# Optimization experiments

Hardware: AMD Instinct MI355X
Metric: run time of the kernel (lower is better)

Reference implementation:

```python
import jax, jax.numpy as jnp
import numpy as np

N_NODES, N_EDGES = 16384, 8192
IN_CH, HID_CH = 256, 256
ALPHA, BETA = -1.5, -0.5


def setup_inputs() -> dict:
    key = jax.random.key(0)
    k1, k2, k3, k4, k5, k6 = jax.random.split(key, 6)
    x_0 = jax.random.normal(k1, (N_NODES, IN_CH), dtype=jnp.float32)
    # binary incidence matrix (n_nodes, n_edges)
    incidence_1 = jax.random.randint(k2, (N_NODES, N_EDGES), 0, 2).astype(jnp.float32)
    # conv weights (torch Conv: x @ W then neighborhood @ .)
    W0 = jax.random.normal(k3, (IN_CH, HID_CH), dtype=jnp.float32) * 0.02
    W1 = jax.random.normal(k4, (HID_CH, HID_CH), dtype=jnp.float32) * 0.02
    # xavier_uniform biases of shape (1, hidden)
    gain = 1.414
    bound = gain * np.sqrt(6.0 / (1 + HID_CH)) * np.sqrt(3.0) / np.sqrt(3.0)  # xavier bound = gain*sqrt(6/(fan_in+fan_out))
    bound = gain * np.sqrt(6.0 / (1 + HID_CH))
    bias_0_to_1 = jax.random.uniform(k5, (1, HID_CH), minval=-bound, maxval=bound, dtype=jnp.float32)
    bias_1_to_0 = jax.random.uniform(k6, (1, HID_CH), minval=-bound, maxval=bound, dtype=jnp.float32)
    return {"x_0": x_0, "incidence_1": incidence_1, "W0": W0, "W1": W1,
            "bias_0_to_1": bias_0_to_1, "bias_1_to_0": bias_1_to_0}


def _normalize_incidence(B1):
    # edge/node cardinalities raised to alpha/beta
    edge_card = jnp.sum(B1, axis=0) ** ALPHA          # (n_edges,)
    node_card = jnp.sum(B1, axis=1) ** BETA           # (n_nodes,)
    mask = (B1 > 0).astype(B1.dtype)
    d0_inv = 1.0 / (mask @ edge_card)                 # (n_nodes,) per-node sum of incident edge_card
    d1_inv = 1.0 / (mask.T @ node_card)               # (n_edges,) per-edge sum of member node_card
    # B1_norm = D0_left^-1 @ B1 @ diag(edge_card)
    B1_norm = d0_inv[:, None] * B1 * edge_card[None, :]
    # B1T_norm = D1_left^-1 @ B1^T @ diag(node_card)
    B1T_norm = d1_inv[:, None] * B1.T * node_card[None, :]
    return B1_norm, B1T_norm


def reference(x_0, incidence_1, W0, W1, bias_0_to_1, bias_1_to_0):
    B1_norm, B1T_norm = _normalize_incidence(incidence_1)
    # node -> edge conv: x_1 = B1T_norm @ (x_0 @ W0) + b01
    x_1 = B1T_norm @ (x_0 @ W0) + bias_0_to_1        # (n_edges, hid)
    # edge -> node conv: x_0 = B1_norm @ (x_1 @ W1) + b10
    x_0_out = B1_norm @ (x_1 @ W1) + bias_1_to_0     # (n_nodes, hid)
    return jax.nn.relu(x_0_out), jax.nn.relu(x_1)
```

## Files before the change

### kernel.cpp

```cpp
#include <hip/hip_runtime.h>
#include <stdint.h>

#define NN 16384
#define NE 8192
#define CH 256
#define MM1_SPLIT 8
#define MM2_SPLIT 4

typedef __attribute__((ext_vector_type(8))) short bf16x8;
typedef __attribute__((ext_vector_type(4))) float f32x4;

__device__ __forceinline__ unsigned short f2bf(float f) {
  unsigned u = __float_as_uint(f);
  u += 0x7FFFu + ((u >> 16) & 1u);
  return (unsigned short)(u >> 16);
}
__device__ __forceinline__ void async_copy16(const void* gptr, void* lptr) {
  __builtin_amdgcn_global_load_lds((const __attribute__((address_space(1))) unsigned int*)gptr,
                                   (__attribute__((address_space(3))) unsigned int*)lptr,
                                   16, 0, 0);
}
__device__ __forceinline__ uint4 expand8(unsigned byte) {
  uint4 aw;
#pragma unroll
  for (int j = 0; j < 4; ++j) {
    unsigned lo = (byte >> (2 * j)) & 1u;
    unsigned hi = (byte >> (2 * j + 1)) & 1u;
    ((unsigned*)&aw)[j] = lo * 0x3F80u + hi * 0x3F800000u;
  }
  return aw;
}

__device__ __forceinline__ void transpose32(unsigned* x) {
  const unsigned masks[5] = {0x0000FFFFu, 0x00FF00FFu, 0x0F0F0F0Fu, 0x33333333u, 0x55555555u};
#pragma unroll
  for (int jj = 0; jj < 5; ++jj) {
    const int j = 16 >> jj;
    const unsigned m = masks[jj];
#pragma unroll
    for (int k = 0; k < 32; ++k) {
      if ((k & j) == 0) {
        unsigned t = ((x[k] >> j) ^ x[k + j]) & m;
        x[k] ^= (t << j);
        x[k + j] ^= t;
      }
    }
  }
}

__global__ void k0_transpose_w(const float* __restrict__ W0, const float* __restrict__ W1,
                               unsigned short* __restrict__ W0T, unsigned short* __restrict__ W1T) {
  const float* W = blockIdx.y ? W1 : W0;
  unsigned short* WT = blockIdx.y ? W1T : W0T;
  int n = blockIdx.x;
  int k = threadIdx.x;
  WT[n * CH + k] = f2bf(W[k * CH + n]);
}

__global__ void k1_pack_card(const float* __restrict__ B1, unsigned* __restrict__ pk1,
                             float* __restrict__ node_card) {
  int n = blockIdx.x;
  int t = threadIdx.x;
  const float4* p = (const float4*)(B1 + (size_t)n * NE + t * 32);
  unsigned w = 0;
#pragma unroll
  for (int jj = 0; jj < 8; ++jj) {
    float4 v = p[jj];
    w |= ((__float_as_uint(v.x) >> 23) & 1u) << (4 * jj);
    w |= ((__float_as_uint(v.y) >> 23) & 1u) << (4 * jj + 1);
    w |= ((__float_as_uint(v.z) >> 23) & 1u) << (4 * jj + 2);
    w |= ((__float_as_uint(v.w) >> 23) & 1u) << (4 * jj + 3);
  }
  pk1[(size_t)n * 256 + t] = w;
  int s = __popc(w);
  __shared__ int red[4];
#pragma unroll
  for (int off = 32; off; off >>= 1) s += __shfl_down(s, off, 64);
  if ((t & 63) == 0) red[t >> 6] = s;
  __syncthreads();
  if (t == 0) {
    float tot = (float)(red[0] + red[1] + red[2] + red[3]);
    node_card[n] = rsqrtf(tot);
  }
}

__global__ __launch_bounds__(256) void k1b_bitT(const unsigned* __restrict__ pk1,
                                                unsigned* __restrict__ pk1T) {
  int bw = blockIdx.x & 127;
  int half = blockIdx.x >> 7;
  int t = threadIdx.x;
  int nt = half * 256 + t;
  unsigned x0[32], x1[32];
#pragma unroll
  for (int r = 0; r < 32; ++r) {
    uint2 v = *(const uint2*)&pk1[(size_t)(nt * 32 + r) * 256 + 2 * bw];
    x0[r] = v.x;
    x1[r] = v.y;
  }
  transpose32(x0);
  transpose32(x1);
  int e0 = bw * 64;
#pragma unroll
  for (int c = 0; c < 32; ++c) {
    pk1T[(size_t)(e0 + c) * 512 + nt] = x0[c];
    pk1T[(size_t)(e0 + 32 + c) * 512 + nt] = x1[c];
  }
}

__global__ void kcs_edge_card(const unsigned* __restrict__ pk1T, float* __restrict__ edge_card) {
  int lane = threadIdx.x & 63;
  int e = blockIdx.x * 4 + (threadIdx.x >> 6);
  const uint4* p = (const uint4*)(pk1T + (size_t)e * 512) + lane * 2;
  uint4 a = p[0], b = p[1];
  int s = __popc(a.x) + __popc(a.y) + __popc(a.z) + __popc(a.w) +
          __popc(b.x) + __popc(b.y) + __popc(b.z) + __popc(b.w);
#pragma unroll
  for (int off = 32; off; off >>= 1) s += __shfl_down(s, off, 64);
  if (lane == 0) {
    float cs = (float)s;
    edge_card[e] = 1.0f / (cs * sqrtf(cs));
  }
}

__global__ __launch_bounds__(256) void k2_y0(const float* __restrict__ X0,
                                             const unsigned short* __restrict__ W0T,
                                             const float* __restrict__ node_card,
                                             unsigned short* __restrict__ y0sT) {
  __shared__ __align__(16) unsigned short a_lds[64 * 32];
  __shared__ __align__(16) unsigned short b_lds[256 * 32];
  const int tid = threadIdx.x;
  const int wave = tid >> 6, lane = tid & 63;
  const int quad = lane >> 4, l15 = lane & 15;
  const int m0 = blockIdx.x * 64;
  const int ar = tid >> 3, ac = (tid & 7) * 4;

  f32x4 acc[4][4];
  const f32x4 fz = {0.f, 0.f, 0.f, 0.f};
#pragma unroll
  for (int i = 0; i < 4; ++i)
#pragma unroll
    for (int j = 0; j < 4; ++j) acc[i][j] = fz;

  for (int k0 = 0; k0 < CH; k0 += 32) {
    __syncthreads();
#pragma unroll
    for (int p = 0; p < 2; ++p) {
      float4 v = *(const float4*)(X0 + (size_t)(m0 + ar + p * 32) * CH + k0 + ac);
      uint2 w;
      w.x = ((unsigned)f2bf(v.x)) | ((unsigned)f2bf(v.y) << 16);
      w.y = ((unsigned)f2bf(v.z)) | ((unsigned)f2bf(v.w) << 16);
      *(uint2*)&a_lds[(ar + p * 32) * 32 + ac] = w;
    }
#pragma unroll
    for (int i = 0; i < 4; ++i) {
      int rowbase = wave * 64 + i * 16;
      const unsigned short* g = W0T + (size_t)(rowbase + (lane >> 2)) * CH + k0 + (lane & 3) * 8;
      async_copy16(g, &b_lds[rowbase * 32]);
    }
    __syncthreads();
    bf16x8 af[4];
#pragma unroll
    for (int i = 0; i < 4; ++i)
      af[i] = *(const bf16x8*)&a_lds[(i * 16 + l15) * 32 + quad * 8];
#pragma unroll
    for (int j = 0; j < 4; ++j) {
      bf16x8 bfr = *(const bf16x8*)&b_lds[(wave * 64 + j * 16 + l15) * 32 + quad * 8];
#pragma unroll
      for (int i = 0; i < 4; ++i)
        acc[i][j] = __builtin_amdgcn_mfma_f32_16x16x32_bf16(af[i], bfr, acc[i][j], 0, 0, 0);
    }
  }
#pragma unroll
  for (int i = 0; i < 4; ++i) {
    int row4 = m0 + i * 16 + quad * 4;
    float4 nc = *(const float4*)(node_card + row4);
#pragma unroll
    for (int j = 0; j < 4; ++j) {
      int col = wave * 64 + j * 16 + l15;
      f32x4 v = acc[i][j];
      ushort4 o;
      o.x = f2bf(v[0] * nc.x);
      o.y = f2bf(v[1] * nc.y);
      o.z = f2bf(v[2] * nc.z);
      o.w = f2bf(v[3] * nc.w);
      *(ushort4*)&y0sT[(size_t)col * NN + row4] = o;
    }
  }
}

__global__ void k2b_aux(const float* __restrict__ node_card, unsigned short* __restrict__ y0sT) {
  int n = blockIdx.x * 256 + threadIdx.x;
  y0sT[(size_t)256 * NN + n] = f2bf(node_card[n]);
}

__global__ __launch_bounds__(512, 4) void mm1_kernel(const unsigned char* __restrict__ pk1T,
                                                     const unsigned short* __restrict__ y0sT,
                                                     float* __restrict__ mm1p,
                                                     float* __restrict__ auxD) {
  __shared__ __align__(16) unsigned short a_lds[2][128 * 40];
  __shared__ __align__(16) unsigned short b_lds[2][272 * 32];
  const int tid = threadIdx.x;
  const int wave = tid >> 6, lane = tid & 63;
  const int quad = lane >> 4, l15 = lane & 15;
  const int wm = wave >> 2, wn = wave & 3;
  const int bid = blockIdx.x;
  const int sp = bid & 7;
  const int m0 = (bid >> 3) * 128;
  const int KS = NN / MM1_SPLIT;
  const int NT = KS / 32;
  const int kbase = sp * KS;

  const int am = tid >> 2;
  const int akg = tid & 3;
  const int ajbs = akg ^ ((am >> 4) & 3);
  const int aoff = am * 40 + ajbs * 8;

  const int brow = lane >> 2;
  const int bcol = (lane & 3) * 8;

  f32x4 acc[4][4];
  const f32x4 fz = {0.f, 0.f, 0.f, 0.f};
#pragma unroll
  for (int i = 0; i < 4; ++i)
#pragma unroll
    for (int j = 0; j < 4; ++j) acc[i][j] = fz;
  float daux = 0.f;

  const unsigned char* agp = pk1T + (size_t)(m0 + am) * (NN / 8) + (kbase >> 3) + akg;
  unsigned ab_cur = agp[0];
  unsigned ab_nxt = agp[4];
  const unsigned char* agq = agp + 8;

#pragma unroll
  for (int i = 0; i < 2; ++i) {
    int rowbase = wave * 32 + i * 16;
    const unsigned short* g = y0sT + (size_t)(rowbase + brow) * NN + kbase + bcol;
    async_copy16(g, &b_lds[0][rowbase * 32]);
  }
  if (wave == 7) {
    const unsigned short* g = y0sT + (size_t)(256 + brow) * NN + kbase + bcol;
    async_copy16(g, &b_lds[0][256 * 32]);
  }
  *(uint4*)&a_lds[0][aoff] = expand8(ab_cur);
  __syncthreads();

  for (int t = 0; t < NT; ++t) {
    const int cur = t & 1;
    unsigned ab_new = 0;
    if (t + 1 < NT) {
      const int k0n = kbase + (t + 1) * 32;
#pragma unroll
      for (int i = 0; i < 2; ++i) {
        int rowbase = wave * 32 + i * 16;
        const unsigned short* g = y0sT + (size_t)(rowbase + brow) * NN + k0n + bcol;
        async_copy16(g, &b_lds[cur ^ 1][rowbase * 32]);
      }
      if (wave == 7) {
        const unsigned short* g = y0sT + (size_t)(256 + brow) * NN + k0n + bcol;
        async_copy16(g, &b_lds[cur ^ 1][256 * 32]);
      }
      *(uint4*)&a_lds[cur ^ 1][aoff] = expand8(ab_nxt);
      if (t + 2 < NT) {
        ab_new = *agq;
        agq += 4;
      }
    }
    {
      bf16x8 nc8 = *(const bf16x8*)&b_lds[cur][256 * 32 + akg * 8];
      float part = 0.f;
#pragma unroll
      for (int j = 0; j < 8; ++j) {
        float ncf = __uint_as_float(((unsigned)(unsigned short)nc8[j]) << 16);
        part += ((ab_cur >> j) & 1u) ? ncf : 0.f;
      }
      daux += part;
    }
    bf16x8 af[4];
#pragma unroll
    for (int i = 0; i < 4; ++i) {
      int m = wm * 64 + i * 16 + l15;
      int jbs = quad ^ i;
      af[i] = *(const bf16x8*)&a_lds[cur][m * 40 + jbs * 8];
    }
#pragma unroll
    for (int j = 0; j < 4; ++j) {
      bf16x8 bfr = *(const bf16x8*)&b_lds[cur][(wn * 64 + j * 16 + l15) * 32 + quad * 8];
#pragma unroll
      for (int i = 0; i < 4; ++i)
        acc[i][j] = __builtin_amdgcn_mfma_f32_16x16x32_bf16(af[i], bfr, acc[i][j], 0, 0, 0);
    }
    __syncthreads();
    ab_cur = ab_nxt;
    ab_nxt = ab_new;
  }
  float* outp = mm1p + (size_t)sp * NE * CH;
#pragma unroll
  for (int i = 0; i < 4; ++i) {
    int row4 = m0 + wm * 64 + i * 16 + quad * 4;
#pragma unroll
    for (int j = 0; j < 4; ++j) {
      int col = wn * 64 + j * 16 + l15;
#pragma unroll
      for (int r = 0; r < 4; ++r) outp[(size_t)(row4 + r) * CH + col] = acc[i][j][r];
    }
  }
  __syncthreads();
  float* dred = (float*)a_lds;
  dred[tid] = daux;
  __syncthreads();
  if (tid < 128) {
    float s = dred[tid * 4] + dred[tid * 4 + 1] + dred[tid * 4 + 2] + dred[tid * 4 + 3];
    auxD[(size_t)sp * NE + m0 + tid] = s;
  }
}

__global__ void k3_edge_final(const float* __restrict__ mm1p, const float* __restrict__ auxD,
                              const float* __restrict__ b01,
                              float* __restrict__ out1, unsigned short* __restrict__ x1bf) {
  int e = blockIdx.x, c = threadIdx.x;
  float ds = 0.f, p = 0.f;
#pragma unroll
  for (int sp = 0; sp < MM1_SPLIT; ++sp) {
    ds += auxD[(size_t)sp * NE + e];
    p += mm1p[(size_t)sp * NE * CH + (size_t)e * CH + c];
  }
  float x1 = p / ds + b01[c];
  out1[(size_t)e * CH + c] = fmaxf(x1, 0.f);
  x1bf[(size_t)e * CH + c] = f2bf(x1);
}

__global__ __launch_bounds__(256) void k5_y1(const unsigned short* __restrict__ x1bf,
                                             const unsigned short* __restrict__ W1T,
                                             const float* __restrict__ edge_card,
                                             unsigned short* __restrict__ y1sT) {
  __shared__ __align__(16) unsigned short a_lds[64 * 32];
  __shared__ __align__(16) unsigned short b_lds[256 * 32];
  const int tid = threadIdx.x;
  const int wave = tid >> 6, lane = tid & 63;
  const int quad = lane >> 4, l15 = lane & 15;
  const int m0 = blockIdx.x * 64;

  f32x4 acc[4][4];
  const f32x4 fz = {0.f, 0.f, 0.f, 0.f};
#pragma unroll
  for (int i = 0; i < 4; ++i)
#pragma unroll
    for (int j = 0; j < 4; ++j) acc[i][j] = fz;

  for (int k0 = 0; k0 < CH; k0 += 32) {
    __syncthreads();
    {
      const unsigned short* g = x1bf + (size_t)(m0 + wave * 16 + (lane >> 2)) * CH + k0 + (lane & 3) * 8;
      async_copy16(g, &a_lds[(wave * 16) * 32]);
    }
#pragma unroll
    for (int i = 0; i < 4; ++i) {
      int rowbase = wave * 64 + i * 16;
      const unsigned short* g = W1T + (size_t)(rowbase + (lane >> 2)) * CH + k0 + (lane & 3) * 8;
      async_copy16(g, &b_lds[rowbase * 32]);
    }
    __syncthreads();
    bf16x8 af[4];
#pragma unroll
    for (int i = 0; i < 4; ++i)
      af[i] = *(const bf16x8*)&a_lds[(i * 16 + l15) * 32 + quad * 8];
#pragma unroll
    for (int j = 0; j < 4; ++j) {
      bf16x8 bfr = *(const bf16x8*)&b_lds[(wave * 64 + j * 16 + l15) * 32 + quad * 8];
#pragma unroll
      for (int i = 0; i < 4; ++i)
        acc[i][j] = __builtin_amdgcn_mfma_f32_16x16x32_bf16(af[i], bfr, acc[i][j], 0, 0, 0);
    }
  }
#pragma unroll
  for (int i = 0; i < 4; ++i) {
    int row4 = m0 + i * 16 + quad * 4;
    float4 ec = *(const float4*)(edge_card + row4);
#pragma unroll
    for (int j = 0; j < 4; ++j) {
      int col = wave * 64 + j * 16 + l15;
      f32x4 v = acc[i][j];
      ushort4 o;
      o.x = f2bf(v[0] * ec.x);
      o.y = f2bf(v[1] * ec.y);
      o.z = f2bf(v[2] * ec.z);
      o.w = f2bf(v[3] * ec.w);
      *(ushort4*)&y1sT[(size_t)col * NE + row4] = o;
    }
  }
}

__global__ void k5b_aux(const float* __restrict__ edge_card, unsigned short* __restrict__ y1sT) {
  int e = blockIdx.x * 256 + threadIdx.x;
  y1sT[(size_t)256 * NE + e] = f2bf(edge_card[e]);
}

__global__ __launch_bounds__(512, 4) void mm2_kernel(const unsigned char* __restrict__ pk1,
                                                     const unsigned short* __restrict__ y1sT,
                                                     float* __restrict__ mm2p,
                                                     float* __restrict__ d0p) {
  __shared__ __align__(16) unsigned short a_lds[2][128 * 40];
  __shared__ __align__(16) unsigned short b_lds[2][272 * 32];
  const int tid = threadIdx.x;
  const int wave = tid >> 6, lane = tid & 63;
  const int quad = lane >> 4, l15 = lane & 15;
  const int wm = wave >> 2, wn = wave & 3;
  const int bid = blockIdx.x;
  const int sp = (bid >> 1) & 3;
  const int m0 = (((bid >> 3) << 1) | (bid & 1)) * 128;
  const int KS = NE / MM2_SPLIT;
  const int NT = KS / 32;
  const int kbase = sp * KS;

  const int am = tid >> 2;
  const int akg = tid & 3;
  const int ajbs = akg ^ ((am >> 4) & 3);
  const int aoff = am * 40 + ajbs * 8;
  const int brow = lane >> 2;
  const int bcol = (lane & 3) * 8;

  f32x4 acc[4][4];
  const f32x4 fz = {0.f, 0.f, 0.f, 0.f};
#pragma unroll
  for (int i = 0; i < 4; ++i)
#pragma unroll
    for (int j = 0; j < 4; ++j) acc[i][j] = fz;
  float daux = 0.f;

  const unsigned char* agp = pk1 + (size_t)(m0 + am) * (NE / 8) + (kbase >> 3) + akg;
  unsigned ab_cur = agp[0];
  unsigned ab_nxt = agp[4];
  const unsigned char* agq = agp + 8;

#pragma unroll
  for (int i = 0; i < 2; ++i) {
    int rowbase = wave * 32 + i * 16;
    const unsigned short* g = y1sT + (size_t)(rowbase + brow) * NE + kbase + bcol;
    async_copy16(g, &b_lds[0][rowbase * 32]);
  }
  if (wave == 7) {
    const unsigned short* g = y1sT + (size_t)(256 + brow) * NE + kbase + bcol;
    async_copy16(g, &b_lds[0][256 * 32]);
  }
  *(uint4*)&a_lds[0][aoff] = expand8(ab_cur);
  __syncthreads();

  for (int t = 0; t < NT; ++t) {
    const int cur = t & 1;
    unsigned ab_new = 0;
    if (t + 1 < NT) {
      const int k0n = kbase + (t + 1) * 32;
#pragma unroll
      for (int i = 0; i < 2; ++i) {
        int rowbase = wave * 32 + i * 16;
        const unsigned short* g = y1sT + (size_t)(rowbase + brow) * NE + k0n + bcol;
        async_copy16(g, &b_lds[cur ^ 1][rowbase * 32]);
      }
      if (wave == 7) {
        const unsigned short* g = y1sT + (size_t)(256 + brow) * NE + k0n + bcol;
        async_copy16(g, &b_lds[cur ^ 1][256 * 32]);
      }
      *(uint4*)&a_lds[cur ^ 1][aoff] = expand8(ab_nxt);
      if (t + 2 < NT) {
        ab_new = *agq;
        agq += 4;
      }
    }
    {
      bf16x8 ec8 = *(const bf16x8*)&b_lds[cur][256 * 32 + akg * 8];
      float part = 0.f;
#pragma unroll
      for (int j = 0; j < 8; ++j) {
        float ecf = __uint_as_float(((unsigned)(unsigned short)ec8[j]) << 16);
        part += ((ab_cur >> j) & 1u) ? ecf : 0.f;
      }
      daux += part;
    }
    bf16x8 af[4];
#pragma unroll
    for (int i = 0; i < 4; ++i) {
      int m = wm * 64 + i * 16 + l15;
      int jbs = quad ^ i;
      af[i] = *(const bf16x8*)&a_lds[cur][m * 40 + jbs * 8];
    }
#pragma unroll
    for (int j = 0; j < 4; ++j) {
      bf16x8 bfr = *(const bf16x8*)&b_lds[cur][(wn * 64 + j * 16 + l15) * 32 + quad * 8];
#pragma unroll
      for (int i = 0; i < 4; ++i)
        acc[i][j] = __builtin_amdgcn_mfma_f32_16x16x32_bf16(af[i], bfr, acc[i][j], 0, 0, 0);
    }
    __syncthreads();
    ab_cur = ab_nxt;
    ab_nxt = ab_new;
  }
  float* outp = mm2p + (size_t)sp * NN * CH;
#pragma unroll
  for (int i = 0; i < 4; ++i) {
    int row4 = m0 + wm * 64 + i * 16 + quad * 4;
#pragma unroll
    for (int j = 0; j < 4; ++j) {
      int col = wn * 64 + j * 16 + l15;
#pragma unroll
      for (int r = 0; r < 4; ++r) outp[(size_t)(row4 + r) * CH + col] = acc[i][j][r];
    }
  }
  __syncthreads();
  float* dred = (float*)a_lds;
  dred[tid] = daux;
  __syncthreads();
  if (tid < 128) {
    float s = dred[tid * 4] + dred[tid * 4 + 1] + dred[tid * 4 + 2] + dred[tid * 4 + 3];
    d0p[(size_t)sp * NN + m0 + tid] = s;
  }
}

__global__ void k6_node_final(const float* __restrict__ mm2p, const float* __restrict__ d0p,
                              const float* __restrict__ b10, float* __restrict__ out0) {
  int n = blockIdx.x, c = threadIdx.x;
  float s = 0.f, d = 0.f;
#pragma unroll
  for (int sp = 0; sp < MM2_SPLIT; ++sp) {
    s += mm2p[(size_t)sp * NN * CH + (size_t)n * CH + c];
    d += d0p[(size_t)sp * NN + n];
  }
  float v = s / d + b10[c];
  out0[(size_t)n * CH + c] = fmaxf(v, 0.f);
}

extern "C" void kernel_launch(void* const* d_in, const int* in_sizes, int n_in,
                              void* d_out, int out_size, void* d_ws, size_t ws_size,
                              hipStream_t stream) {
  const float* x0 = (const float*)d_in[0];
  const float* B1 = (const float*)d_in[1];
  const float* W0 = (const float*)d_in[2];
  const float* W1 = (const float*)d_in[3];
  const float* b01 = (const float*)d_in[4];
  const float* b10 = (const float*)d_in[5];
  float* out0 = (float*)d_out;
  float* out1 = out0 + (size_t)NN * CH;

  char* ws = (char*)d_ws;
  size_t off = 0;
  auto take = [&](size_t bytes) {
    void* p = ws + off;
    off += (bytes + 255) & ~(size_t)255;
    return p;
  };
  unsigned short* y0sT = (unsigned short*)take((size_t)272 * NN * 2);
  unsigned short* y1sT = (unsigned short*)take((size_t)272 * NE * 2);
  unsigned short* x1bf = (unsigned short*)take((size_t)NE * CH * 2);
  float* mm1p = (float*)take((size_t)MM1_SPLIT * NE * CH * 4);
  float* mm2p = mm1p;
  float* node_card = (float*)take((size_t)NN * 4);
  float* edge_card = (float*)take((size_t)NE * 4);
  float* auxD = (float*)take((size_t)MM1_SPLIT * NE * 4);
  float* d0p = (float*)take((size_t)MM2_SPLIT * NN * 4);
  unsigned short* W0T = (unsigned short*)take((size_t)CH * CH * 2);
  unsigned short* W1T = (unsigned short*)take((size_t)CH * CH * 2);
  unsigned* pk1 = (unsigned*)take((size_t)NN * 256 * 4);
  unsigned* pk1T = (unsigned*)take((size_t)NE * 512 * 4);
  (void)ws_size; (void)in_sizes; (void)n_in; (void)out_size;

  k0_transpose_w<<<dim3(256, 2), 256, 0, stream>>>(W0, W1, W0T, W1T);
  k1_pack_card<<<NN, 256, 0, stream>>>(B1, pk1, node_card);
  k1b_bitT<<<256, 256, 0, stream>>>(pk1, pk1T);
  kcs_edge_card<<<NE / 4, 256, 0, stream>>>(pk1T, edge_card);
  k2_y0<<<NN / 64, 256, 0, stream>>>(x0, W0T, node_card, y0sT);
  k2b_aux<<<NN / 256, 256, 0, stream>>>(node_card, y0sT);
  mm1_kernel<<<512, 512, 0, stream>>>((const unsigned char*)pk1T, y0sT, mm1p, auxD);
  k3_edge_final<<<NE, 256, 0, stream>>>(mm1p, auxD, b01, out1, x1bf);
  k5_y1<<<NE / 64, 256, 0, stream>>>(x1bf, W1T, edge_card, y1sT);
  k5b_aux<<<NE / 256, 256, 0, stream>>>(edge_card, y1sT);
  mm2_kernel<<<512, 512, 0, stream>>>((const unsigned char*)pk1, y1sT, mm2p, d0p);
  k6_node_final<<<NN, 256, 0, stream>>>(mm2p, d0p, b10, out0);
}
```

Before: 974.0 us.

## Move degree normalizer sums out of GEMM loops into dedicated bitmask kernels

Computes the per-edge (d1) and per-node (d0) normalizer sums in two standalone popcount/bitmask reduction kernels instead of accumulating them inside the mm1/mm2 main loops via an extra 16-row aux slab. The GEMM kernels lose the wave-7 extra async copy, the per-iteration masked accumulation and the final LDS reduction, and the finalize kernels read one normalizer value instead of summing split partials. It also halves the M tile of the y0/y1 projection GEMMs to launch more blocks, and changes the A-fragment swizzle index. The cost is extra small launches and extra passes over the packed incidence bits.

```diff
diff --git a/kernel.cpp b/kernel.cpp
--- a/kernel.cpp
+++ b/kernel.cpp
@@ -107,49 +107,127 @@
   }
 }
 
-__global__ void kcs_edge_card(const unsigned* __restrict__ pk1T, float* __restrict__ edge_card) {
-  int lane = threadIdx.x & 63;
-  int e = blockIdx.x * 4 + (threadIdx.x >> 6);
-  const uint4* p = (const uint4*)(pk1T + (size_t)e * 512) + lane * 2;
-  uint4 a = p[0], b = p[1];
-  int s = __popc(a.x) + __popc(a.y) + __popc(a.z) + __popc(a.w) +
-          __popc(b.x) + __popc(b.y) + __popc(b.z) + __popc(b.w);
-#pragma unroll
-  for (int off = 32; off; off >>= 1) s += __shfl_down(s, off, 64);
-  if (lane == 0) {
-    float cs = (float)s;
-    edge_card[e] = 1.0f / (cs * sqrtf(cs));
-  }
+__global__ __launch_bounds__(256) void ke_edge(const unsigned* __restrict__ pk1T,
+                                               const float* __restrict__ node_card,
+                                               float* __restrict__ edge_card,
+                                               float* __restrict__ d1) {
+  const int t = threadIdx.x;
+  const int e0 = blockIdx.x * 4;
+  unsigned w[4][2];
+#pragma unroll
+  for (int r = 0; r < 4; ++r) {
+    w[r][0] = pk1T[(size_t)(e0 + r) * 512 + t];
+    w[r][1] = pk1T[(size_t)(e0 + r) * 512 + 256 + t];
+  }
+  float wsum[4] = {0.f, 0.f, 0.f, 0.f};
+  int cnt[4];
+#pragma unroll
+  for (int r = 0; r < 4; ++r) cnt[r] = __popc(w[r][0]) + __popc(w[r][1]);
+  const float4* nc0 = (const float4*)(node_card + (size_t)t * 32);
+  const float4* nc1 = (const float4*)(node_card + ((size_t)t + 256) * 32);
+#pragma unroll
+  for (int h = 0; h < 2; ++h) {
+    const float4* ncp = h ? nc1 : nc0;
+#pragma unroll
+    for (int q = 0; q < 8; ++q) {
+      float4 v = ncp[q];
+#pragma unroll
+      for (int r = 0; r < 4; ++r) {
+        unsigned ww = w[r][h];
+        wsum[r] += ((ww >> (4 * q)) & 1u) ? v.x : 0.f;
+        wsum[r] += ((ww >> (4 * q + 1)) & 1u) ? v.y : 0.f;
+        wsum[r] += ((ww >> (4 * q + 2)) & 1u) ? v.z : 0.f;
+        wsum[r] += ((ww >> (4 * q + 3)) & 1u) ? v.w : 0.f;
+      }
+    }
+  }
+#pragma unroll
+  for (int off = 32; off; off >>= 1)
+#pragma unroll
+    for (int r = 0; r < 4; ++r) {
+      wsum[r] += __shfl_down(wsum[r], off, 64);
+      cnt[r] += __shfl_down(cnt[r], off, 64);
+    }
+  __shared__ float redW[4][4];
+  __shared__ int redC[4][4];
+  int wave = t >> 6, lane = t & 63;
+  if (lane == 0)
+#pragma unroll
+    for (int r = 0; r < 4; ++r) {
+      redW[wave][r] = wsum[r];
+      redC[wave][r] = cnt[r];
+    }
+  __syncthreads();
+  if (t < 4) {
+    float s = redW[0][t] + redW[1][t] + redW[2][t] + redW[3][t];
+    float c = (float)(redC[0][t] + redC[1][t] + redC[2][t] + redC[3][t]);
+    d1[e0 + t] = s;
+    edge_card[e0 + t] = 1.0f / (c * sqrtf(c));
+  }
+}
+
+__global__ __launch_bounds__(256) void kd0_node(const unsigned* __restrict__ pk1,
+                                                const float* __restrict__ edge_card,
+                                                float* __restrict__ d0) {
+  const int t = threadIdx.x;
+  const int n0 = blockIdx.x * 4;
+  unsigned w[4];
+#pragma unroll
+  for (int r = 0; r < 4; ++r) w[r] = pk1[(size_t)(n0 + r) * 256 + t];
+  float wsum[4] = {0.f, 0.f, 0.f, 0.f};
+  const float4* ecp = (const float4*)(edge_card + (size_t)t * 32);
+#pragma unroll
+  for (int q = 0; q < 8; ++q) {
+    float4 v = ecp[q];
+#pragma unroll
+    for (int r = 0; r < 4; ++r) {
+      unsigned ww = w[r];
+      wsum[r] += ((ww >> (4 * q)) & 1u) ? v.x : 0.f;
+      wsum[r] += ((ww >> (4 * q + 1)) & 1u) ? v.y : 0.f;
+      wsum[r] += ((ww >> (4 * q + 2)) & 1u) ? v.z : 0.f;
+      wsum[r] += ((ww >> (4 * q + 3)) & 1u) ? v.w : 0.f;
+    }
+  }
+#pragma unroll
+  for (int off = 32; off; off >>= 1)
+#pragma unroll
+    for (int r = 0; r < 4; ++r) wsum[r] += __shfl_down(wsum[r], off, 64);
+  __shared__ float redW[4][4];
+  int wave = t >> 6, lane = t & 63;
+  if (lane == 0)
+#pragma unroll
+    for (int r = 0; r < 4; ++r) redW[wave][r] = wsum[r];
+  __syncthreads();
+  if (t < 4) d0[n0 + t] = redW[0][t] + redW[1][t] + redW[2][t] + redW[3][t];
 }
 
 __global__ __launch_bounds__(256) void k2_y0(const float* __restrict__ X0,
                                              const unsigned short* __restrict__ W0T,
                                              const float* __restrict__ node_card,
                                              unsigned short* __restrict__ y0sT) {
-  __shared__ __align__(16) unsigned short a_lds[64 * 32];
+  __shared__ __align__(16) unsigned short a_lds[32 * 32];
   __shared__ __align__(16) unsigned short b_lds[256 * 32];
   const int tid = threadIdx.x;
   const int wave = tid >> 6, lane = tid & 63;
   const int quad = lane >> 4, l15 = lane & 15;
-  const int m0 = blockIdx.x * 64;
+  const int m0 = blockIdx.x * 32;
   const int ar = tid >> 3, ac = (tid & 7) * 4;
 
-  f32x4 acc[4][4];
+  f32x4 acc[2][4];
   const f32x4 fz = {0.f, 0.f, 0.f, 0.f};
 #pragma unroll
-  for (int i = 0; i < 4; ++i)
+  for (int i = 0; i < 2; ++i)
 #pragma unroll
     for (int j = 0; j < 4; ++j) acc[i][j] = fz;
 
   for (int k0 = 0; k0 < CH; k0 += 32) {
     __syncthreads();
-#pragma unroll
-    for (int p = 0; p < 2; ++p) {
-      float4 v = *(const float4*)(X0 + (size_t)(m0 + ar + p * 32) * CH + k0 + ac);
+    {
+      float4 v = *(const float4*)(X0 + (size_t)(m0 + ar) * CH + k0 + ac);
       uint2 w;
       w.x = ((unsigned)f2bf(v.x)) | ((unsigned)f2bf(v.y) << 16);
       w.y = ((unsigned)f2bf(v.z)) | ((unsigned)f2bf(v.w) << 16);
-      *(uint2*)&a_lds[(ar + p * 32) * 32 + ac] = w;
+      *(uint2*)&a_lds[ar * 32 + ac] = w;
     }
 #pragma unroll
     for (int i = 0; i < 4; ++i) {
@@ -158,20 +236,20 @@
       async_copy16(g, &b_lds[rowbase * 32]);
     }
     __syncthreads();
-    bf16x8 af[4];
-#pragma unroll
-    for (int i = 0; i < 4; ++i)
+    bf16x8 af[2];
+#pragma unroll
+    for (int i = 0; i < 2; ++i)
       af[i] = *(const bf16x8*)&a_lds[(i * 16 + l15) * 32 + quad * 8];
 #pragma unroll
     for (int j = 0; j < 4; ++j) {
       bf16x8 bfr = *(const bf16x8*)&b_lds[(wave * 64 + j * 16 + l15) * 32 + quad * 8];
 #pragma unroll
-      for (int i = 0; i < 4; ++i)
+      for (int i = 0; i < 2; ++i)
         acc[i][j] = __builtin_amdgcn_mfma_f32_16x16x32_bf16(af[i], bfr, acc[i][j], 0, 0, 0);
     }
   }
 #pragma unroll
-  for (int i = 0; i < 4; ++i) {
+  for (int i = 0; i < 2; ++i) {
     int row4 = m0 + i * 16 + quad * 4;
     float4 nc = *(const float4*)(node_card + row4);
 #pragma unroll
@@ -188,17 +266,11 @@
   }
 }
 
-__global__ void k2b_aux(const float* __restrict__ node_card, unsigned short* __restrict__ y0sT) {
-  int n = blockIdx.x * 256 + threadIdx.x;
-  y0sT[(size_t)256 * NN + n] = f2bf(node_card[n]);
-}
-
 __global__ __launch_bounds__(512, 4) void mm1_kernel(const unsigned char* __restrict__ pk1T,
                                                      const unsigned short* __restrict__ y0sT,
-                                                     float* __restrict__ mm1p,
-                                                     float* __restrict__ auxD) {
+                                                     float* __restrict__ mm1p) {
   __shared__ __align__(16) unsigned short a_lds[2][128 * 40];
-  __shared__ __align__(16) unsigned short b_lds[2][272 * 32];
+  __shared__ __align__(16) unsigned short b_lds[2][256 * 32];
   const int tid = threadIdx.x;
   const int wave = tid >> 6, lane = tid & 63;
   const int quad = lane >> 4, l15 = lane & 15;
@@ -214,7 +286,6 @@
   const int akg = tid & 3;
   const int ajbs = akg ^ ((am >> 4) & 3);
   const int aoff = am * 40 + ajbs * 8;
-
   const int brow = lane >> 2;
   const int bcol = (lane & 3) * 8;
 
@@ -224,7 +295,6 @@
   for (int i = 0; i < 4; ++i)
 #pragma unroll
     for (int j = 0; j < 4; ++j) acc[i][j] = fz;
-  float daux = 0.f;
 
   const unsigned char* agp = pk1T + (size_t)(m0 + am) * (NN / 8) + (kbase >> 3) + akg;
   unsigned ab_cur = agp[0];
@@ -236,10 +306,6 @@
     int rowbase = wave * 32 + i * 16;
     const unsigned short* g = y0sT + (size_t)(rowbase + brow) * NN + kbase + bcol;
     async_copy16(g, &b_lds[0][rowbase * 32]);
-  }
-  if (wave == 7) {
-    const unsigned short* g = y0sT + (size_t)(256 + brow) * NN + kbase + bcol;
-    async_copy16(g, &b_lds[0][256 * 32]);
   }
   *(uint4*)&a_lds[0][aoff] = expand8(ab_cur);
   __syncthreads();
@@ -254,10 +320,6 @@
         int rowbase = wave * 32 + i * 16;
         const unsigned short* g = y0sT + (size_t)(rowbase + brow) * NN + k0n + bcol;
         async_copy16(g, &b_lds[cur ^ 1][rowbase * 32]);
-      }
-      if (wave == 7) {
-        const unsigned short* g = y0sT + (size_t)(256 + brow) * NN + k0n + bcol;
-        async_copy16(g, &b_lds[cur ^ 1][256 * 32]);
       }
       *(uint4*)&a_lds[cur ^ 1][aoff] = expand8(ab_nxt);
       if (t + 2 < NT) {
@@ -265,21 +327,11 @@
         agq += 4;
       }
     }
-    {
-      bf16x8 nc8 = *(const bf16x8*)&b_lds[cur][256 * 32 + akg * 8];
-      float part = 0.f;
-#pragma unroll
-      for (int j = 0; j < 8; ++j) {
-        float ncf = __uint_as_float(((unsigned)(unsigned short)nc8[j]) << 16);
-        part += ((ab_cur >> j) & 1u) ? ncf : 0.f;
-      }
-      daux += part;
-    }
     bf16x8 af[4];
 #pragma unroll
     for (int i = 0; i < 4; ++i) {
       int m = wm * 64 + i * 16 + l15;
-      int jbs = quad ^ i;
+      int jbs = quad ^ ((m >> 4) & 3);
       af[i] = *(const bf16x8*)&a_lds[cur][m * 40 + jbs * 8];
     }
 #pragma unroll
@@ -304,27 +356,17 @@
       for (int r = 0; r < 4; ++r) outp[(size_t)(row4 + r) * CH + col] = acc[i][j][r];
     }
   }
-  __syncthreads();
-  float* dred = (float*)a_lds;
-  dred[tid] = daux;
-  __syncthreads();
-  if (tid < 128) {
-    float s = dred[tid * 4] + dred[tid * 4 + 1] + dred[tid * 4 + 2] + dred[tid * 4 + 3];
-    auxD[(size_t)sp * NE + m0 + tid] = s;
-  }
-}
-
-__global__ void k3_edge_final(const float* __restrict__ mm1p, const float* __restrict__ auxD,
+}
+
+__global__ void k3_edge_final(const float* __restrict__ mm1p, const float* __restrict__ d1,
                               const float* __restrict__ b01,
                               float* __restrict__ out1, unsigned short* __restrict__ x1bf) {
   int e = blockIdx.x, c = threadIdx.x;
-  float ds = 0.f, p = 0.f;
-#pragma unroll
-  for (int sp = 0; sp < MM1_SPLIT; ++sp) {
-    ds += auxD[(size_t)sp * NE + e];
+  float p = 0.f;
+#pragma unroll
+  for (int sp = 0; sp < MM1_SPLIT; ++sp)
     p += mm1p[(size_t)sp * NE * CH + (size_t)e * CH + c];
-  }
-  float x1 = p / ds + b01[c];
+  float x1 = p / d1[e] + b01[c];
   out1[(size_t)e * CH + c] = fmaxf(x1, 0.f);
   x1bf[(size_t)e * CH + c] = f2bf(x1);
 }
@@ -333,23 +375,23 @@
                                              const unsigned short* __restrict__ W1T,
                                              const float* __restrict__ edge_card,
                                              unsigned short* __restrict__ y1sT) {
-  __shared__ __align__(16) unsigned short a_lds[64 * 32];
+  __shared__ __align__(16) unsigned short a_lds[32 * 32];
   __shared__ __align__(16) unsigned short b_lds[256 * 32];
   const int tid = threadIdx.x;
   const int wave = tid >> 6, lane = tid & 63;
   const int quad = lane >> 4, l15 = lane & 15;
-  const int m0 = blockIdx.x * 64;
-
-  f32x4 acc[4][4];
+  const int m0 = blockIdx.x * 32;
+
+  f32x4 acc[2][4];
   const f32x4 fz = {0.f, 0.f, 0.f, 0.f};
 #pragma unroll
-  for (int i = 0; i < 4; ++i)
+  for (int i = 0; i < 2; ++i)
 #pragma unroll
     for (int j = 0; j < 4; ++j) acc[i][j] = fz;
 
   for (int k0 = 0; k0 < CH; k0 += 32) {
     __syncthreads();
-    {
+    if (wave < 2) {
       const unsigned short* g = x1bf + (size_t)(m0 + wave * 16 + (lane >> 2)) * CH + k0 + (lane & 3) * 8;
       async_copy16(g, &a_lds[(wave * 16) * 32]);
     }
@@ -360,20 +402,20 @@
       async_copy16(g, &b_lds[rowbase * 32]);
     }
     __syncthreads();
-    bf16x8 af[4];
-#pragma unroll
-    for (int i = 0; i < 4; ++i)
+    bf16x8 af[2];
+#pragma unroll
+    for (int i = 0; i < 2; ++i)
       af[i] = *(const bf16x8*)&a_lds[(i * 16 + l15) * 32 + quad * 8];
 #pragma unroll
     for (int j = 0; j < 4; ++j) {
       bf16x8 bfr = *(const bf16x8*)&b_lds[(wave * 64 + j * 16 + l15) * 32 + quad * 8];
 #pragma unroll
-      for (int i = 0; i < 4; ++i)
+      for (int i = 0; i < 2; ++i)
         acc[i][j] = __builtin_amdgcn_mfma_f32_16x16x32_bf16(af[i], bfr, acc[i][j], 0, 0, 0);
     }
   }
 #pragma unroll
-  for (int i = 0; i < 4; ++i) {
+  for (int i = 0; i < 2; ++i) {
     int row4 = m0 + i * 16 + quad * 4;
     float4 ec = *(const float4*)(edge_card + row4);
 #pragma unroll
@@ -390,17 +432,11 @@
   }
 }
 
-__global__ void k5b_aux(const float* __restrict__ edge_card, unsigned short* __restrict__ y1sT) {
-  int e = blockIdx.x * 256 + threadIdx.x;
-  y1sT[(size_t)256 * NE + e] = f2bf(edge_card[e]);
-}
-
 __global__ __launch_bounds__(512, 4) void mm2_kernel(const unsigned char* __restrict__ pk1,
                                                      const unsigned short* __restrict__ y1sT,
-                                                     float* __restrict__ mm2p,
-                                                     float* __restrict__ d0p) {
+                                                     float* __restrict__ mm2p) {
   __shared__ __align__(16) unsigned short a_lds[2][128 * 40];
-  __shared__ __align__(16) unsigned short b_lds[2][272 * 32];
+  __shared__ __align__(16) unsigned short b_lds[2][256 * 32];
   const int tid = threadIdx.x;
   const int wave = tid >> 6, lane = tid & 63;
   const int quad = lane >> 4, l15 = lane & 15;
@@ -425,7 +461,6 @@
   for (int i = 0; i < 4; ++i)
 #pragma unroll
     for (int j = 0; j < 4; ++j) acc[i][j] = fz;
-  float daux = 0.f;
 
   const unsigned char* agp = pk1 + (size_t)(m0 + am) * (NE / 8) + (kbase >> 3) + akg;
   unsigned ab_cur = agp[0];
@@ -437,10 +472,6 @@
     int rowbase = wave * 32 + i * 16;
     const unsigned short* g = y1sT + (size_t)(rowbase + brow) * NE + kbase + bcol;
     async_copy16(g, &b_lds[0][rowbase * 32]);
-  }
-  if (wave == 7) {
-    const unsigned short* g = y1sT + (size_t)(256 + brow) * NE + kbase + bcol;
-    async_copy16(g, &b_lds[0][256 * 32]);
   }
   *(uint4*)&a_lds[0][aoff] = expand8(ab_cur);
   __syncthreads();
@@ -455,10 +486,6 @@
         int rowbase = wave * 32 + i * 16;
         const unsigned short* g = y1sT + (size_t)(rowbase + brow) * NE + k0n + bcol;
         async_copy16(g, &b_lds[cur ^ 1][rowbase * 32]);
-      }
-      if (wave == 7) {
-        const unsigned short* g = y1sT + (size_t)(256 + brow) * NE + k0n + bcol;
-        async_copy16(g, &b_lds[cur ^ 1][256 * 32]);
       }
       *(uint4*)&a_lds[cur ^ 1][aoff] = expand8(ab_nxt);
       if (t + 2 < NT) {
@@ -466,21 +493,11 @@
         agq += 4;
       }
     }
-    {
-      bf16x8 ec8 = *(const bf16x8*)&b_lds[cur][256 * 32 + akg * 8];
-      float part = 0.f;
-#pragma unroll
-      for (int j = 0; j < 8; ++j) {
-        float ecf = __uint_as_float(((unsigned)(unsigned short)ec8[j]) << 16);
-        part += ((ab_cur >> j) & 1u) ? ecf : 0.f;
-      }
-      daux += part;
-    }
     bf16x8 af[4];
 #pragma unroll
     for (int i = 0; i < 4; ++i) {
       int m = wm * 64 + i * 16 + l15;
-      int jbs = quad ^ i;
+      int jbs = quad ^ ((m >> 4) & 3);
       af[i] = *(const bf16x8*)&a_lds[cur][m * 40 + jbs * 8];
     }
 #pragma unroll
@@ -505,26 +522,16 @@
       for (int r = 0; r < 4; ++r) outp[(size_t)(row4 + r) * CH + col] = acc[i][j][r];
     }
   }
-  __syncthreads();
-  float* dred = (float*)a_lds;
-  dred[tid] = daux;
-  __syncthreads();
-  if (tid < 128) {
-    float s = dred[tid * 4] + dred[tid * 4 + 1] + dred[tid * 4 + 2] + dred[tid * 4 + 3];
-    d0p[(size_t)sp * NN + m0 + tid] = s;
-  }
-}
-
-__global__ void k6_node_final(const float* __restrict__ mm2p, const float* __restrict__ d0p,
+}
+
+__global__ void k6_node_final(const float* __restrict__ mm2p, const float* __restrict__ d0,
                               const float* __restrict__ b10, float* __restrict__ out0) {
   int n = blockIdx.x, c = threadIdx.x;
-  float s = 0.f, d = 0.f;
-#pragma unroll
-  for (int sp = 0; sp < MM2_SPLIT; ++sp) {
+  float s = 0.f;
+#pragma unroll
+  for (int sp = 0; sp < MM2_SPLIT; ++sp)
     s += mm2p[(size_t)sp * NN * CH + (size_t)n * CH + c];
-    d += d0p[(size_t)sp * NN + n];
-  }
-  float v = s / d + b10[c];
+  float v = s / d0[n] + b10[c];
   out0[(size_t)n * CH + c] = fmaxf(v, 0.f);
 }
 
@@ -547,15 +554,15 @@
     off += (bytes + 255) & ~(size_t)255;
     return p;
   };
-  unsigned short* y0sT = (unsigned short*)take((size_t)272 * NN * 2);
-  unsigned short* y1sT = (unsigned short*)take((size_t)272 * NE * 2);
+  unsigned short* y0sT = (unsigned short*)take((size_t)256 * NN * 2);
+  unsigned short* y1sT = (unsigned short*)take((size_t)256 * NE * 2);
   unsigned short* x1bf = (unsigned short*)take((size_t)NE * CH * 2);
   float* mm1p = (float*)take((size_t)MM1_SPLIT * NE * CH * 4);
   float* mm2p = mm1p;
   float* node_card = (float*)take((size_t)NN * 4);
   float* edge_card = (float*)take((size_t)NE * 4);
-  float* auxD = (float*)take((size_t)MM1_SPLIT * NE * 4);
-  float* d0p = (float*)take((size_t)MM2_SPLIT * NN * 4);
+  float* d1 = (float*)take((size_t)NE * 4);
+  float* d0 = (float*)take((size_t)NN * 4);
   unsigned short* W0T = (unsigned short*)take((size_t)CH * CH * 2);
   unsigned short* W1T = (unsigned short*)take((size_t)CH * CH * 2);
   unsigned* pk1 = (unsigned*)take((size_t)NN * 256 * 4);
@@ -565,13 +572,12 @@
   k0_transpose_w<<<dim3(256, 2), 256, 0, stream>>>(W0, W1, W0T, W1T);
   k1_pack_card<<<NN, 256, 0, stream>>>(B1, pk1, node_card);
   k1b_bitT<<<256, 256, 0, stream>>>(pk1, pk1T);
-  kcs_edge_card<<<NE / 4, 256, 0, stream>>>(pk1T, edge_card);
-  k2_y0<<<NN / 64, 256, 0, stream>>>(x0, W0T, node_card, y0sT);
-  k2b_aux<<<NN / 256, 256, 0, stream>>>(node_card, y0sT);
-  mm1_kernel<<<512, 512, 0, stream>>>((const unsigned char*)pk1T, y0sT, mm1p, auxD);
-  k3_edge_final<<<NE, 256, 0, stream>>>(mm1p, auxD, b01, out1, x1bf);
-  k5_y1<<<NE / 64, 256, 0, stream>>>(x1bf, W1T, edge_card, y1sT);
-  k5b_aux<<<NE / 256, 256, 0, stream>>>(edge_card, y1sT);
-  mm2_kernel<<<512, 512, 0, stream>>>((const unsigned char*)pk1, y1sT, mm2p, d0p);
-  k6_node_final<<<NN, 256, 0, stream>>>(mm2p, d0p, b10, out0);
-}
+  ke_edge<<<NE / 4, 256, 0, stream>>>(pk1T, node_card, edge_card, d1);
+  kd0_node<<<NN / 4, 256, 0, stream>>>(pk1, edge_card, d0);
+  k2_y0<<<NN / 32, 256, 0, stream>>>(x0, W0T, node_card, y0sT);
+  mm1_kernel<<<512, 512, 0, stream>>>((const unsigned char*)pk1T, y0sT, mm1p);
+  k3_edge_final<<<NE, 256, 0, stream>>>(mm1p, d1, b01, out1, x1bf);
+  k5_y1<<<NE / 32, 256, 0, stream>>>(x1bf, W1T, edge_card, y1sT);
+  mm2_kernel<<<512, 512, 0, stream>>>((const unsigned char*)pk1, y1sT, mm2p);
+  k6_node_final<<<NN, 256, 0, stream>>>(mm2p, d0, b10, out0);
+}
```

New measurement: 956.0 us. No clear change (-1.8%).
